# Kernel tuning notes

Hardware: AMD Instinct MI355X
Metric: run time of the kernel (lower is better)

The kernel has to match this reference:

```python
import jax, jax.numpy as jnp
import numpy as np
from jax import lax

DN = ('NCHW', 'OIHW', 'NCHW')
NUM_HEADS = 6


def _conv1x1(x, w):
    return lax.conv_general_dilated(x, w, (1, 1), 'VALID', dimension_numbers=DN)


def _dwconv3x3(x, w):
    # depthwise 3x3, groups == channels, padding 1
    return lax.conv_general_dilated(x, w, (1, 1), ((1, 1), (1, 1)),
                                    dimension_numbers=DN,
                                    feature_group_count=w.shape[0])


def setup_inputs() -> dict:
    key = jax.random.key(0)
    ks = jax.random.split(key, 7)
    b, dim, h, w = 4, 192, 128, 128
    inp = {
        'x': jax.random.normal(ks[0], (b, dim, h, w), jnp.float32),
        'ref': jax.random.normal(ks[1], (b, dim, h, w), jnp.float32),
        'w_qkv': jax.random.normal(ks[2], (dim * 3, dim, 1, 1), jnp.float32) * 0.05,
        'w_dw': jax.random.normal(ks[3], (dim * 3, 1, 3, 3), jnp.float32) * 0.1,
        'w_proj': jax.random.normal(ks[4], (dim, dim, 1, 1), jnp.float32) * 0.05,
        'temperature': jnp.ones((NUM_HEADS, 1, 1), jnp.float32),
        'attn_w': 0.2 * jnp.ones((4,), jnp.float32),
    }
    return inp


def reference(x, ref, w_qkv, w_dw, w_proj, temperature, attn_w):
    b, c, h, w = x.shape
    heads = NUM_HEADS
    C = c // heads  # per-head channel dim
    hw = h * w

    qkv = _dwconv3x3(_conv1x1(x, w_qkv), w_dw)        # [b, 3c, h, w]
    ref_qkv = _dwconv3x3(_conv1x1(ref, w_qkv), w_dw)  # shared weights

    q_shared = qkv[:, :c]            # q from x
    k_shared = ref_qkv[:, c:2 * c]   # k from ref
    v_shared = ref_qkv[:, 2 * c:]    # v from ref

    def to_heads(t):  # [b, c, h, w] -> [b, head, C, hw]
        return t.reshape(b, heads, C, hw)

    q = to_heads(q_shared)
    k = to_heads(k_shared)
    v = to_heads(v_shared)

    # L2-normalize along token dim (last axis)
    q = q / jnp.maximum(jnp.linalg.norm(q, axis=-1, keepdims=True), 1e-12)
    k = k / jnp.maximum(jnp.linalg.norm(k, axis=-1, keepdims=True), 1e-12)

    # channel-wise attention: [b, head, C, C]
    attn = jnp.einsum('bhcn,bhdn->bhcd', q, k) * temperature

    ks_list = [int(C / 2), int(C * 2 / 3), int(C * 3 / 4), int(C * 4 / 5)]
    neg_inf = jnp.asarray(-jnp.inf, attn.dtype)

    out = 0.0
    for i, ki in enumerate(ks_list):
        vals = lax.top_k(attn, ki)[0]            # [b, head, C, ki]
        thr = vals[..., -1:]                     # k-th largest per row
        a = jnp.where(attn >= thr, attn, neg_inf)
        a = jax.nn.softmax(a, axis=-1)
        out = out + attn_w[i] * jnp.einsum('bhcd,bhdn->bhcn', a, v)

    out = out.reshape(b, c, h, w)
    return _conv1x1(out, w_proj)
```

## Files before the change

kernel.cpp:

```cpp
#include <hip/hip_runtime.h>
#include <cstdint>
#include <cstddef>

typedef unsigned short u16;
typedef unsigned int u32;
typedef __attribute__((ext_vector_type(2))) float f32x2;
typedef __attribute__((ext_vector_type(4))) float f32x4;
typedef __attribute__((ext_vector_type(8))) short short8;
typedef __attribute__((ext_vector_type(2))) u32 u32x2;
typedef __attribute__((ext_vector_type(4))) u32 u32x4;

#define DEV static __device__ __forceinline__
#define HW 16384

DEV u16 f2bf(float f) {
  u32 u = __float_as_uint(f);
  u = (u + 0x7fffu + ((u >> 16) & 1u)) >> 16;
  return (u16)u;
}
DEV float bf2f(u16 h) { return __uint_as_float(((u32)h) << 16); }

DEV u32 packsplit(float f) {
  u16 h = f2bf(f);
  u16 l = f2bf(f - bf2f(h));
  return (u32)h | ((u32)l << 16);
}
DEV void unpack8(const u32* w, short8& hi, short8& lo) {
  #pragma unroll
  for (int i = 0; i < 8; ++i) {
    hi[i] = (short)(u16)w[i];
    lo[i] = (short)(u16)(w[i] >> 16);
  }
}
DEV void mfma3(f32x4& acc, short8 ah, short8 al, short8 bh, short8 bl) {
  acc = __builtin_amdgcn_mfma_f32_16x16x32_bf16(ah, bh, acc, 0, 0, 0);
  acc = __builtin_amdgcn_mfma_f32_16x16x32_bf16(ah, bl, acc, 0, 0, 0);
  acc = __builtin_amdgcn_mfma_f32_16x16x32_bf16(al, bh, acc, 0, 0, 0);
}


__global__ __launch_bounds__(256) void ksplit2(const float* __restrict__ in,
                                               u16* __restrict__ oh,
                                               u16* __restrict__ ol, int n) {
  int i = blockIdx.x * 256 + threadIdx.x;
  if (i >= n) return;
  int R = i / 192, K = i % 192;
  int halfblk = R / 96, rem = R % 96, mf = rem >> 4, r = rem & 15;
  int p = K >> 5, kk = K & 31, g = kk >> 3, j = kk & 7;
  size_t o16 = (((size_t)halfblk * 6 + p) * 6 + mf) * 512 + (size_t)(g * 16 + r) * 8 + j;
  float f = in[i];
  u16 h = f2bf(f);
  oh[o16] = h;
  ol[o16] = f2bf(f - bf2f(h));
}

template<int ABATCH, int BPACKED>
__global__ __launch_bounds__(512, 4) void gemm8(const u16* __restrict__ Afh,
                                                const u16* __restrict__ Afl,
                                                const u32* __restrict__ B0,
                                                const u32* __restrict__ B1,
                                                float* __restrict__ C0,
                                                float* __restrict__ C1) {
  __shared__ u32 Bs[2][128 * 34];
  const int t = threadIdx.x, lane = t & 63, wid = t >> 6;
  const int b = blockIdx.z, n0 = blockIdx.x * 128, y = blockIdx.y;
  const u32* Bb = (y == 0 ? B0 : B1) + (size_t)b * 192 * (size_t)HW;
  float* Cb = (y == 0) ? (C0 + (size_t)b * 192 * (size_t)HW)
                       : (C1 + ((size_t)b * 384 + (size_t)(y - 1) * 192) * (size_t)HW);
  const int wr = wid >> 2, wc = wid & 3;
  const int g = lane >> 4, r16 = lane & 15;
  const int bk = t >> 4;
  const int bn = t & 15;
  const int halfblk = (ABATCH ? b : y) * 2 + wr;
  const u16* Ah_w = Afh + (size_t)halfblk * 36 * 512 + (size_t)lane * 8;
  const u16* Al_w = Afl + (size_t)halfblk * 36 * 512 + (size_t)lane * 8;
  f32x4 acc[6][2] = {};

  u32 Breg[8], Bnext[8];
  #pragma unroll
  for (int j = 0; j < 8; ++j)
    Breg[j] = Bb[(size_t)bk * HW + n0 + bn + 16 * j];
  #pragma unroll 1
  for (int p = 0; p < 6; ++p) {
    u32* bufc = Bs[p & 1];
    #pragma unroll
    for (int j = 0; j < 8; ++j)
      bufc[(bn + 16 * j) * 34 + bk] =
          BPACKED ? Breg[j] : packsplit(__uint_as_float(Breg[j]));
    if (p < 5) {
      #pragma unroll
      for (int j = 0; j < 8; ++j)
        Bnext[j] = Bb[(size_t)((p + 1) * 32 + bk) * HW + n0 + bn + 16 * j];
    }
    __syncthreads();
    short8 bh[2], bl[2];
    #pragma unroll
    for (int nf = 0; nf < 2; ++nf) {
      u32 bw[8];
      const u32* bp = &bufc[(wc * 32 + nf * 16 + r16) * 34 + g * 8];
      *(u32x2*)&bw[0] = *(const u32x2*)&bp[0];
      *(u32x2*)&bw[2] = *(const u32x2*)&bp[2];
      *(u32x2*)&bw[4] = *(const u32x2*)&bp[4];
      *(u32x2*)&bw[6] = *(const u32x2*)&bp[6];
      unpack8(bw, bh[nf], bl[nf]);
    }
    #pragma unroll
    for (int mf = 0; mf < 6; ++mf) {
      const int fo = (p * 6 + mf) << 9;
      short8 ah = *(const short8*)(Ah_w + fo);
      short8 al = *(const short8*)(Al_w + fo);
      #pragma unroll
      for (int nf = 0; nf < 2; ++nf) {
        acc[mf][nf] = __builtin_amdgcn_mfma_f32_16x16x32_bf16(ah, bh[nf], acc[mf][nf], 0, 0, 0);
        acc[mf][nf] = __builtin_amdgcn_mfma_f32_16x16x32_bf16(ah, bl[nf], acc[mf][nf], 0, 0, 0);
        acc[mf][nf] = __builtin_amdgcn_mfma_f32_16x16x32_bf16(al, bh[nf], acc[mf][nf], 0, 0, 0);
      }
    }
    #pragma unroll
    for (int j = 0; j < 8; ++j) Breg[j] = Bnext[j];
  }
  #pragma unroll
  for (int mf = 0; mf < 6; ++mf)
    #pragma unroll
    for (int nf = 0; nf < 2; ++nf)
      #pragma unroll
      for (int rr = 0; rr < 4; ++rr)
        Cb[(size_t)(wr * 96 + mf * 16 + g * 4 + rr) * HW + n0 + wc * 32 + nf * 16 + r16] =
            acc[mf][nf][rr];
}

template<int SSQ>
__global__ __launch_bounds__(512) void k2_dw(const float* __restrict__ Tin, int cstIn,
                                             const float* __restrict__ wdw, int wco,
                                             u32* __restrict__ O,
                                             float* __restrict__ ssq, int sspath) {
  const int rt = blockIdx.x, cg = blockIdx.y, b = blockIdx.z;
  const int t = threadIdx.x, lane = t & 63, w = t >> 6;
  __shared__ float In[8][10][132];
  for (int idx = t; idx < 10400; idx += 512) {
    int ch = idx / 1300, rem = idx % 1300;
    int r = rem / 130, ci = rem % 130;
    int gr = rt * 8 + r - 1, gc = ci - 1;
    float v = 0.f;
    if (gr >= 0 && gr < 128 && gc >= 0 && gc < 128)
      v = Tin[((size_t)b * cstIn + cg * 8 + ch) * HW + gr * 128 + gc];
    In[ch][r][ci] = v;
  }
  float wv[9];
  #pragma unroll
  for (int j = 0; j < 9; ++j) wv[j] = wdw[(size_t)(wco + cg * 8 + w) * 9 + j];
  __syncthreads();
  float s = 0.f;
  u32* Op = O + ((size_t)b * 192 + cg * 8 + w) * HW + rt * 8 * 128 + 2 * lane;
  #pragma unroll
  for (int i = 0; i < 8; ++i) {
    float a0 = 0.f, a1 = 0.f;
    #pragma unroll
    for (int dr = 0; dr < 3; ++dr) {
      f32x2 u0 = *(const f32x2*)&In[w][i + dr][2 * lane];
      f32x2 u1 = *(const f32x2*)&In[w][i + dr][2 * lane + 2];
      a0 += wv[dr * 3] * u0[0] + wv[dr * 3 + 1] * u0[1] + wv[dr * 3 + 2] * u1[0];
      a1 += wv[dr * 3] * u0[1] + wv[dr * 3 + 1] * u1[0] + wv[dr * 3 + 2] * u1[1];
    }
    u32x2 o = {packsplit(a0), packsplit(a1)};
    *(u32x2*)&Op[(size_t)i * 128] = o;
    if (SSQ) s += a0 * a0 + a1 * a1;
  }
  if (SSQ) {
    #pragma unroll
    for (int off = 32; off; off >>= 1) s += __shfl_down(s, off);
    if (lane == 0) ssq[(((size_t)b * 2 + sspath) * 192 + cg * 8 + w) * 16 + rt] = s;
  }
}

__global__ __launch_bounds__(256) void k3_gram(const u32* __restrict__ q,
                                               const u32* __restrict__ k,
                                               float* __restrict__ gp) {
  const int ck = blockIdx.x, bh = blockIdx.y;
  const int b = bh / 6, h = bh % 6;
  const int t = threadIdx.x, lane = t & 63, wid = t >> 6;
  const int r16 = lane & 15, g = lane >> 4;
  const int chunk = ck * 4 + wid;
  const size_t rbase = ((size_t)b * 192 + h * 32 + r16) * HW;
  const u32* qp = q + rbase;
  const u32* kp = k + rbase;
  __shared__ float red[4][1024];
  f32x4 acc[2][2] = {};
  #pragma unroll 1
  for (int s = 0; s < 8; ++s) {
    int n = chunk * 256 + s * 32 + g * 8;
    u32 wq0[8], wq1[8], wk0[8], wk1[8];
    *(u32x4*)&wq0[0] = *(const u32x4*)&qp[n];
    *(u32x4*)&wq0[4] = *(const u32x4*)&qp[n + 4];
    *(u32x4*)&wq1[0] = *(const u32x4*)&qp[(size_t)16 * HW + n];
    *(u32x4*)&wq1[4] = *(const u32x4*)&qp[(size_t)16 * HW + n + 4];
    *(u32x4*)&wk0[0] = *(const u32x4*)&kp[n];
    *(u32x4*)&wk0[4] = *(const u32x4*)&kp[n + 4];
    *(u32x4*)&wk1[0] = *(const u32x4*)&kp[(size_t)16 * HW + n];
    *(u32x4*)&wk1[4] = *(const u32x4*)&kp[(size_t)16 * HW + n + 4];
    short8 a0h, a0l, a1h, a1l, b0h, b0l, b1h, b1l;
    unpack8(wq0, a0h, a0l);
    unpack8(wq1, a1h, a1l);
    unpack8(wk0, b0h, b0l);
    unpack8(wk1, b1h, b1l);
    mfma3(acc[0][0], a0h, a0l, b0h, b0l);
    mfma3(acc[0][1], a0h, a0l, b1h, b1l);
    mfma3(acc[1][0], a1h, a1l, b0h, b0l);
    mfma3(acc[1][1], a1h, a1l, b1h, b1l);
  }
  #pragma unroll
  for (int mf = 0; mf < 2; ++mf)
    #pragma unroll
    for (int nf = 0; nf < 2; ++nf)
      #pragma unroll
      for (int rr = 0; rr < 4; ++rr)
        red[wid][(mf * 16 + g * 4 + rr) * 32 + nf * 16 + r16] = acc[mf][nf][rr];
  __syncthreads();
  float* outp = gp + ((size_t)bh * 16 + ck) * 1024;
  #pragma unroll
  for (int e = t; e < 1024; e += 256)
    outp[e] = red[0][e] + red[1][e] + red[2][e] + red[3][e];
}

__global__ __launch_bounds__(512) void k4_comb(const float* __restrict__ gp,
                                               const float* __restrict__ ssq,
                                               const float* __restrict__ temp,
                                               const float* __restrict__ aw,
                                               const float* __restrict__ wproj,
                                               u16* __restrict__ mfh,
                                               u16* __restrict__ mfl) {
  const int bh = blockIdx.x, b = bh / 6, h = bh % 6;
  const int t = threadIdx.x;
  __shared__ float Gs[1024];
  __shared__ float Acm[1024];
  __shared__ float Wp[192 * 32];
  __shared__ float nq[32], nk[32];
  #pragma unroll
  for (int i = 0; i < 3; ++i) {
    int idx = t + i * 512;
    int row = idx >> 3, c4 = (idx & 7) << 2;
    *(f32x4*)&Wp[row * 32 + c4] = *(const f32x4*)&wproj[(size_t)row * 192 + h * 32 + c4];
  }
  {
    const float* p = gp + (size_t)bh * 16 * 1024 + 2 * t;
    f32x2 s = {};
    #pragma unroll
    for (int ch = 0; ch < 16; ++ch) {
      f32x2 v = *(const f32x2*)&p[(size_t)ch * 1024];
      s[0] += v[0]; s[1] += v[1];
    }
    *(f32x2*)&Gs[2 * t] = s;
  }
  if (t < 64) {
    int c = t & 31, pk = t >> 5;
    const float* sp = ssq + (((size_t)b * 2 + pk) * 192 + h * 32 + c) * 16;
    f32x4 s4 = {};
    #pragma unroll
    for (int i = 0; i < 4; ++i) {
      f32x4 v = *(const f32x4*)&sp[4 * i];
      s4[0] += v[0]; s4[1] += v[1]; s4[2] += v[2]; s4[3] += v[3];
    }
    float nr = fmaxf(sqrtf(s4[0] + s4[1] + s4[2] + s4[3]), 1e-12f);
    if (pk == 0) nq[c] = nr; else nk[c] = nr;
  }
  __syncthreads();
  const float T = temp[h];
  {
    int c = (2 * t) >> 5;
    f32x2 v = *(const f32x2*)&Gs[2 * t];
    float inq = T / nq[c];
    v[0] = v[0] * inq / nk[(2 * t) & 31];
    v[1] = v[1] * inq / nk[(2 * t + 1) & 31];
    __syncthreads();
    *(f32x2*)&Gs[2 * t] = v;
  }
  __syncthreads();
  const float aw0 = aw[0], aw1 = aw[1], aw2 = aw[2], aw3 = aw[3];
  const int half = t >> 5, d = t & 31;
  #pragma unroll
  for (int it = 0; it < 2; ++it) {
    const int c = it * 16 + half;
    const float v = Gs[c * 32 + d];
    int cnt = 0;
    #pragma unroll
    for (int dd = 0; dd < 32; ++dd) cnt += (Gs[c * 32 + dd] >= v) ? 1 : 0;
    float c0 = v;
    float c1 = (cnt >= 16) ? v : -3.0e38f;
    float c2 = (cnt >= 21) ? v : -3.0e38f;
    float c3 = (cnt >= 24) ? v : -3.0e38f;
    float c4 = (cnt >= 25) ? v : -3.0e38f;
    #pragma unroll
    for (int off = 16; off; off >>= 1) {
      c0 = fmaxf(c0, __shfl_xor(c0, off));
      c1 = fmaxf(c1, __shfl_xor(c1, off));
      c2 = fmaxf(c2, __shfl_xor(c2, off));
      c3 = fmaxf(c3, __shfl_xor(c3, off));
      c4 = fmaxf(c4, __shfl_xor(c4, off));
    }
    const float m = c0;
    const float ex = expf(v - m);
    float z1 = (v >= c1) ? ex : 0.f;
    float z2 = (v >= c2) ? ex : 0.f;
    float z3 = (v >= c3) ? ex : 0.f;
    float z4 = (v >= c4) ? ex : 0.f;
    #pragma unroll
    for (int off = 16; off; off >>= 1) {
      z1 += __shfl_xor(z1, off);
      z2 += __shfl_xor(z2, off);
      z3 += __shfl_xor(z3, off);
      z4 += __shfl_xor(z4, off);
    }
    float a = 0.f;
    a += (v >= c1) ? aw0 * ex / z1 : 0.f;
    a += (v >= c2) ? aw1 * ex / z2 : 0.f;
    a += (v >= c3) ? aw2 * ex / z3 : 0.f;
    a += (v >= c4) ? aw3 * ex / z4 : 0.f;
    Acm[c * 32 + d] = a;
  }
  __syncthreads();
  #pragma unroll
  for (int i = 0; i < 12; ++i) {
    int idx = t + i * 512;
    int co = idx >> 5, dd = idx & 31;
    float s = 0.f;
    #pragma unroll
    for (int c = 0; c < 32; ++c) s += Wp[co * 32 + c] * Acm[c * 32 + dd];
    int wr2 = co / 96, rem = co % 96, mf = rem >> 4, r = rem & 15;
    int lane2 = ((dd >> 3) << 4) + r, j = dd & 7;
    size_t o16 = ((((size_t)b * 2 + wr2) * 6 + h) * 6 + mf) * 512 + (size_t)lane2 * 8 + j;
    u16 hh = f2bf(s);
    mfh[o16] = hh;
    mfl[o16] = f2bf(s - bf2f(hh));
  }
}

extern "C" void kernel_launch(void* const* d_in, const int* in_sizes, int n_in,
                              void* d_out, int out_size, void* d_ws, size_t ws_size,
                              hipStream_t stream) {
  const float* x     = (const float*)d_in[0];
  const float* ref   = (const float*)d_in[1];
  const float* wqkv  = (const float*)d_in[2];
  const float* wdw   = (const float*)d_in[3];
  const float* wproj = (const float*)d_in[4];
  const float* temp  = (const float*)d_in[5];
  const float* aw    = (const float*)d_in[6];
  float* out = (float*)d_out;
  char* ws = (char*)d_ws;

  const size_t S = (size_t)4 * 192 * HW * 4;
  float* Ckv = (float*)(ws);
  float* Cq  = (float*)(ws + 2 * S);
  u32*   qpk = (u32*)(ws + 3 * S);
  char*  p5  = ws + 4 * S;
  float* gp  = (float*)(p5);
  float* ssq = (float*)(p5 + 1572864);
  u16*   afh = (u16*)(p5 + 1572864 + 98304);
  u16*   afl = (u16*)(p5 + 1572864 + 98304 + 221184);
  u16*   mfh = (u16*)(p5 + 1572864 + 98304 + 2 * 221184);
  u16*   mfl = (u16*)(p5 + 1572864 + 98304 + 2 * 221184 + 294912);
  u32*   kpk = (u32*)Cq;
  u32*   vpk = qpk;

  ksplit2<<<dim3(432), 256, 0, stream>>>(wqkv, afh, afl, 576 * 192);
  gemm8<0, 0><<<dim3(128, 3, 4), 512, 0, stream>>>(afh, afl, (const u32*)x,
                                                   (const u32*)ref, Cq, Ckv);
  k2_dw<1><<<dim3(16, 24, 4), 512, 0, stream>>>(Cq, 192, wdw, 0, qpk, ssq, 0);
  k2_dw<1><<<dim3(16, 24, 4), 512, 0, stream>>>(Ckv, 384, wdw, 192, kpk, ssq, 1);
  k3_gram<<<dim3(16, 24), 256, 0, stream>>>(qpk, kpk, gp);
  k2_dw<0><<<dim3(16, 24, 4), 512, 0, stream>>>(Ckv + (size_t)192 * HW, 384, wdw, 384,
                                                vpk, nullptr, 2);
  k4_comb<<<dim3(24), 512, 0, stream>>>(gp, ssq, temp, aw, wproj, mfh, mfl);
  gemm8<1, 1><<<dim3(128, 1, 4), 512, 0, stream>>>(mfh, mfl, vpk, vpk, out, out);
}
```

Before: 224.3 us.

## Load B fragments directly from global memory, dropping the LDS staging in the GEMM

After: 241.3 us. 7.6% more time.

```diff
diff --git a/kernel.cpp b/kernel.cpp
--- a/kernel.cpp
+++ b/kernel.cpp
@@ -55,13 +55,12 @@
 }
 
 template<int ABATCH, int BPACKED>
-__global__ __launch_bounds__(512, 4) void gemm8(const u16* __restrict__ Afh,
+__global__ __launch_bounds__(512, 4) void gemm9(const u16* __restrict__ Afh,
                                                 const u16* __restrict__ Afl,
                                                 const u32* __restrict__ B0,
                                                 const u32* __restrict__ B1,
                                                 float* __restrict__ C0,
                                                 float* __restrict__ C1) {
-  __shared__ u32 Bs[2][128 * 34];
   const int t = threadIdx.x, lane = t & 63, wid = t >> 6;
   const int b = blockIdx.z, n0 = blockIdx.x * 128, y = blockIdx.y;
   const u32* Bb = (y == 0 ? B0 : B1) + (size_t)b * 192 * (size_t)HW;
@@ -69,55 +68,48 @@
                        : (C1 + ((size_t)b * 384 + (size_t)(y - 1) * 192) * (size_t)HW);
   const int wr = wid >> 2, wc = wid & 3;
   const int g = lane >> 4, r16 = lane & 15;
-  const int bk = t >> 4;
-  const int bn = t & 15;
   const int halfblk = (ABATCH ? b : y) * 2 + wr;
   const u16* Ah_w = Afh + (size_t)halfblk * 36 * 512 + (size_t)lane * 8;
   const u16* Al_w = Afl + (size_t)halfblk * 36 * 512 + (size_t)lane * 8;
+  const u32* Bp0 = Bb + (size_t)(g * 8) * HW + n0 + wc * 32 + r16;
+  const u32* Bp1 = Bp0 + 16;
   f32x4 acc[6][2] = {};
 
-  u32 Breg[8], Bnext[8];
-  #pragma unroll
-  for (int j = 0; j < 8; ++j)
-    Breg[j] = Bb[(size_t)bk * HW + n0 + bn + 16 * j];
+  u32 bw0[8], bw1[8], bn0[8], bn1[8];
+  #pragma unroll
+  for (int j = 0; j < 8; ++j) {
+    bw0[j] = Bp0[(size_t)j * HW];
+    bw1[j] = Bp1[(size_t)j * HW];
+  }
   #pragma unroll 1
   for (int p = 0; p < 6; ++p) {
-    u32* bufc = Bs[p & 1];
-    #pragma unroll
-    for (int j = 0; j < 8; ++j)
-      bufc[(bn + 16 * j) * 34 + bk] =
-          BPACKED ? Breg[j] : packsplit(__uint_as_float(Breg[j]));
     if (p < 5) {
       #pragma unroll
-      for (int j = 0; j < 8; ++j)
-        Bnext[j] = Bb[(size_t)((p + 1) * 32 + bk) * HW + n0 + bn + 16 * j];
-    }
-    __syncthreads();
-    short8 bh[2], bl[2];
-    #pragma unroll
-    for (int nf = 0; nf < 2; ++nf) {
-      u32 bw[8];
-      const u32* bp = &bufc[(wc * 32 + nf * 16 + r16) * 34 + g * 8];
-      *(u32x2*)&bw[0] = *(const u32x2*)&bp[0];
-      *(u32x2*)&bw[2] = *(const u32x2*)&bp[2];
-      *(u32x2*)&bw[4] = *(const u32x2*)&bp[4];
-      *(u32x2*)&bw[6] = *(const u32x2*)&bp[6];
-      unpack8(bw, bh[nf], bl[nf]);
-    }
+      for (int j = 0; j < 8; ++j) {
+        bn0[j] = Bp0[(size_t)((p + 1) * 32 + j) * HW];
+        bn1[j] = Bp1[(size_t)((p + 1) * 32 + j) * HW];
+      }
+    }
+    if (!BPACKED) {
+      #pragma unroll
+      for (int j = 0; j < 8; ++j) {
+        bw0[j] = packsplit(__uint_as_float(bw0[j]));
+        bw1[j] = packsplit(__uint_as_float(bw1[j]));
+      }
+    }
+    short8 bh0, bl0, bh1, bl1;
+    unpack8(bw0, bh0, bl0);
+    unpack8(bw1, bh1, bl1);
     #pragma unroll
     for (int mf = 0; mf < 6; ++mf) {
       const int fo = (p * 6 + mf) << 9;
       short8 ah = *(const short8*)(Ah_w + fo);
       short8 al = *(const short8*)(Al_w + fo);
-      #pragma unroll
-      for (int nf = 0; nf < 2; ++nf) {
-        acc[mf][nf] = __builtin_amdgcn_mfma_f32_16x16x32_bf16(ah, bh[nf], acc[mf][nf], 0, 0, 0);
-        acc[mf][nf] = __builtin_amdgcn_mfma_f32_16x16x32_bf16(ah, bl[nf], acc[mf][nf], 0, 0, 0);
-        acc[mf][nf] = __builtin_amdgcn_mfma_f32_16x16x32_bf16(al, bh[nf], acc[mf][nf], 0, 0, 0);
-      }
-    }
-    #pragma unroll
-    for (int j = 0; j < 8; ++j) Breg[j] = Bnext[j];
+      mfma3(acc[mf][0], ah, al, bh0, bl0);
+      mfma3(acc[mf][1], ah, al, bh1, bl1);
+    }
+    #pragma unroll
+    for (int j = 0; j < 8; ++j) { bw0[j] = bn0[j]; bw1[j] = bn1[j]; }
   }
   #pragma unroll
   for (int mf = 0; mf < 6; ++mf)
@@ -362,7 +354,7 @@
   u32*   vpk = qpk;
 
   ksplit2<<<dim3(432), 256, 0, stream>>>(wqkv, afh, afl, 576 * 192);
-  gemm8<0, 0><<<dim3(128, 3, 4), 512, 0, stream>>>(afh, afl, (const u32*)x,
+  gemm9<0, 0><<<dim3(128, 3, 4), 512, 0, stream>>>(afh, afl, (const u32*)x,
                                                    (const u32*)ref, Cq, Ckv);
   k2_dw<1><<<dim3(16, 24, 4), 512, 0, stream>>>(Cq, 192, wdw, 0, qpk, ssq, 0);
   k2_dw<1><<<dim3(16, 24, 4), 512, 0, stream>>>(Ckv, 384, wdw, 192, kpk, ssq, 1);
@@ -370,5 +362,5 @@
   k2_dw<0><<<dim3(16, 24, 4), 512, 0, stream>>>(Ckv + (size_t)192 * HW, 384, wdw, 384,
                                                 vpk, nullptr, 2);
   k4_comb<<<dim3(24), 512, 0, stream>>>(gp, ssq, temp, aw, wproj, mfh, mfl);
-  gemm8<1, 1><<<dim3(128, 1, 4), 512, 0, stream>>>(mfh, mfl, vpk, vpk, out, out);
-}
+  gemm9<1, 1><<<dim3(128, 1, 4), 512, 0, stream>>>(mfh, mfl, vpk, vpk, out, out);
+}
```

## Use per-wave B staging in GEMM and merge q/k depthwise launches

Applied to the files above, without the earlier changes.

After: 254.3 us. 1.13x slower.

```diff
diff --git a/kernel.cpp b/kernel.cpp
--- a/kernel.cpp
+++ b/kernel.cpp
@@ -55,53 +55,47 @@
 }
 
 template<int ABATCH, int BPACKED>
-__global__ __launch_bounds__(512, 4) void gemm8(const u16* __restrict__ Afh,
-                                                const u16* __restrict__ Afl,
-                                                const u32* __restrict__ B0,
-                                                const u32* __restrict__ B1,
-                                                float* __restrict__ C0,
-                                                float* __restrict__ C1) {
-  __shared__ u32 Bs[2][128 * 34];
+__global__ __launch_bounds__(256, 4) void gemm12(const u16* __restrict__ Afh,
+                                                 const u16* __restrict__ Afl,
+                                                 const u32* __restrict__ B0,
+                                                 const u32* __restrict__ B1,
+                                                 float* __restrict__ C0,
+                                                 float* __restrict__ C1) {
+  __shared__ u32 Bls[4][2][1152];
   const int t = threadIdx.x, lane = t & 63, wid = t >> 6;
-  const int b = blockIdx.z, n0 = blockIdx.x * 128, y = blockIdx.y;
+  const int b = blockIdx.z, y = blockIdx.y;
+  const int wr = wid >> 1, wc = wid & 1;
+  const int n0w = blockIdx.x * 64 + wc * 32;
   const u32* Bb = (y == 0 ? B0 : B1) + (size_t)b * 192 * (size_t)HW;
   float* Cb = (y == 0) ? (C0 + (size_t)b * 192 * (size_t)HW)
                        : (C1 + ((size_t)b * 384 + (size_t)(y - 1) * 192) * (size_t)HW);
-  const int wr = wid >> 2, wc = wid & 3;
   const int g = lane >> 4, r16 = lane & 15;
-  const int bk = t >> 4;
-  const int bn = t & 15;
   const int halfblk = (ABATCH ? b : y) * 2 + wr;
   const u16* Ah_w = Afh + (size_t)halfblk * 36 * 512 + (size_t)lane * 8;
   const u16* Al_w = Afl + (size_t)halfblk * 36 * 512 + (size_t)lane * 8;
+  const int kk = lane >> 1, bhalf = lane & 1;
+  const u32* Bsrc = Bb + (size_t)kk * HW + n0w + 16 * bhalf;
   f32x4 acc[6][2] = {};
 
-  u32 Breg[8], Bnext[8];
-  #pragma unroll
-  for (int j = 0; j < 8; ++j)
-    Breg[j] = Bb[(size_t)bk * HW + n0 + bn + 16 * j];
-  #pragma unroll 1
+  #pragma unroll
   for (int p = 0; p < 6; ++p) {
-    u32* bufc = Bs[p & 1];
-    #pragma unroll
-    for (int j = 0; j < 8; ++j)
-      bufc[(bn + 16 * j) * 34 + bk] =
-          BPACKED ? Breg[j] : packsplit(__uint_as_float(Breg[j]));
-    if (p < 5) {
+    u32* sl = &Bls[wid][p & 1][0];
+    #pragma unroll
+    for (int j = 0; j < 4; ++j) {
+      u32x4 v = *(const u32x4*)(Bsrc + (size_t)(p * 32) * HW + 4 * j);
       #pragma unroll
-      for (int j = 0; j < 8; ++j)
-        Bnext[j] = Bb[(size_t)((p + 1) * 32 + bk) * HW + n0 + bn + 16 * j];
-    }
-    __syncthreads();
+      for (int i = 0; i < 4; ++i) {
+        u32 pw = BPACKED ? v[i] : packsplit(__uint_as_float(v[i]));
+        sl[(16 * bhalf + 4 * j + i) * 36 + kk] = pw;
+      }
+    }
     short8 bh[2], bl[2];
     #pragma unroll
     for (int nf = 0; nf < 2; ++nf) {
       u32 bw[8];
-      const u32* bp = &bufc[(wc * 32 + nf * 16 + r16) * 34 + g * 8];
-      *(u32x2*)&bw[0] = *(const u32x2*)&bp[0];
-      *(u32x2*)&bw[2] = *(const u32x2*)&bp[2];
-      *(u32x2*)&bw[4] = *(const u32x2*)&bp[4];
-      *(u32x2*)&bw[6] = *(const u32x2*)&bp[6];
+      const u32* rp = &sl[(nf * 16 + r16) * 36 + g * 8];
+      *(u32x4*)&bw[0] = *(const u32x4*)&rp[0];
+      *(u32x4*)&bw[4] = *(const u32x4*)&rp[4];
       unpack8(bw, bh[nf], bl[nf]);
     }
     #pragma unroll
@@ -109,15 +103,9 @@
       const int fo = (p * 6 + mf) << 9;
       short8 ah = *(const short8*)(Ah_w + fo);
       short8 al = *(const short8*)(Al_w + fo);
-      #pragma unroll
-      for (int nf = 0; nf < 2; ++nf) {
-        acc[mf][nf] = __builtin_amdgcn_mfma_f32_16x16x32_bf16(ah, bh[nf], acc[mf][nf], 0, 0, 0);
-        acc[mf][nf] = __builtin_amdgcn_mfma_f32_16x16x32_bf16(ah, bl[nf], acc[mf][nf], 0, 0, 0);
-        acc[mf][nf] = __builtin_amdgcn_mfma_f32_16x16x32_bf16(al, bh[nf], acc[mf][nf], 0, 0, 0);
-      }
-    }
-    #pragma unroll
-    for (int j = 0; j < 8; ++j) Breg[j] = Bnext[j];
+      mfma3(acc[mf][0], ah, al, bh[0], bl[0]);
+      mfma3(acc[mf][1], ah, al, bh[1], bl[1]);
+    }
   }
   #pragma unroll
   for (int mf = 0; mf < 6; ++mf)
@@ -125,27 +113,48 @@
     for (int nf = 0; nf < 2; ++nf)
       #pragma unroll
       for (int rr = 0; rr < 4; ++rr)
-        Cb[(size_t)(wr * 96 + mf * 16 + g * 4 + rr) * HW + n0 + wc * 32 + nf * 16 + r16] =
+        Cb[(size_t)(wr * 96 + mf * 16 + g * 4 + rr) * HW + n0w + nf * 16 + r16] =
             acc[mf][nf][rr];
 }
 
-template<int SSQ>
-__global__ __launch_bounds__(512) void k2_dw(const float* __restrict__ Tin, int cstIn,
-                                             const float* __restrict__ wdw, int wco,
-                                             u32* __restrict__ O,
-                                             float* __restrict__ ssq, int sspath) {
-  const int rt = blockIdx.x, cg = blockIdx.y, b = blockIdx.z;
+DEV void k2_stage(const float* __restrict__ src, int rt, int w, int lane,
+                  float (*In)[10][132]) {
+  #pragma unroll
+  for (int r = 0; r < 10; ++r) {
+    int gr = rt * 8 + r - 1;
+    bool rowok = (gr >= 0) && (gr < 128);
+    const float* rsrc = src + (size_t)gr * 128;
+    #pragma unroll
+    for (int j = 0; j < 2; ++j) {
+      int ci = j * 64 + lane;
+      int gc = ci - 1;
+      float v = (rowok && gc >= 0) ? rsrc[gc] : 0.f;
+      In[w][r][ci] = v;
+    }
+    if (lane < 2) {
+      float v = (rowok && lane == 0) ? rsrc[127] : 0.f;
+      In[w][r][128 + lane] = v;
+    }
+  }
+}
+
+__global__ __launch_bounds__(512) void k2qk(const float* __restrict__ Cq,
+                                            const float* __restrict__ Ckv,
+                                            const float* __restrict__ wdw,
+                                            u32* __restrict__ qpk,
+                                            u32* __restrict__ kpk,
+                                            float* __restrict__ ssq) {
+  const int rt = blockIdx.x, cgy = blockIdx.y, b = blockIdx.z;
   const int t = threadIdx.x, lane = t & 63, w = t >> 6;
+  const int isK = cgy >= 24;
+  const int cg = isK ? cgy - 24 : cgy;
+  const int cstIn = isK ? 384 : 192;
+  const int wco = isK ? 192 : 0;
+  const float* Tin = isK ? Ckv : Cq;
+  u32* O = isK ? kpk : qpk;
+  const int sspath = isK;
   __shared__ float In[8][10][132];
-  for (int idx = t; idx < 10400; idx += 512) {
-    int ch = idx / 1300, rem = idx % 1300;
-    int r = rem / 130, ci = rem % 130;
-    int gr = rt * 8 + r - 1, gc = ci - 1;
-    float v = 0.f;
-    if (gr >= 0 && gr < 128 && gc >= 0 && gc < 128)
-      v = Tin[((size_t)b * cstIn + cg * 8 + ch) * HW + gr * 128 + gc];
-    In[ch][r][ci] = v;
-  }
+  k2_stage(Tin + ((size_t)b * cstIn + cg * 8 + w) * HW, rt, w, lane, In);
   float wv[9];
   #pragma unroll
   for (int j = 0; j < 9; ++j) wv[j] = wdw[(size_t)(wco + cg * 8 + w) * 9 + j];
@@ -164,12 +173,37 @@
     }
     u32x2 o = {packsplit(a0), packsplit(a1)};
     *(u32x2*)&Op[(size_t)i * 128] = o;
-    if (SSQ) s += a0 * a0 + a1 * a1;
-  }
-  if (SSQ) {
-    #pragma unroll
-    for (int off = 32; off; off >>= 1) s += __shfl_down(s, off);
-    if (lane == 0) ssq[(((size_t)b * 2 + sspath) * 192 + cg * 8 + w) * 16 + rt] = s;
+    s += a0 * a0 + a1 * a1;
+  }
+  #pragma unroll
+  for (int off = 32; off; off >>= 1) s += __shfl_down(s, off);
+  if (lane == 0) ssq[(((size_t)b * 2 + sspath) * 192 + cg * 8 + w) * 16 + rt] = s;
+}
+
+__global__ __launch_bounds__(512) void k2v(const float* __restrict__ Tin,
+                                           const float* __restrict__ wdw,
+                                           u32* __restrict__ O) {
+  const int rt = blockIdx.x, cg = blockIdx.y, b = blockIdx.z;
+  const int t = threadIdx.x, lane = t & 63, w = t >> 6;
+  __shared__ float In[8][10][132];
+  k2_stage(Tin + ((size_t)b * 384 + cg * 8 + w) * HW, rt, w, lane, In);
+  float wv[9];
+  #pragma unroll
+  for (int j = 0; j < 9; ++j) wv[j] = wdw[(size_t)(384 + cg * 8 + w) * 9 + j];
+  __syncthreads();
+  u32* Op = O + ((size_t)b * 192 + cg * 8 + w) * HW + rt * 8 * 128 + 2 * lane;
+  #pragma unroll
+  for (int i = 0; i < 8; ++i) {
+    float a0 = 0.f, a1 = 0.f;
+    #pragma unroll
+    for (int dr = 0; dr < 3; ++dr) {
+      f32x2 u0 = *(const f32x2*)&In[w][i + dr][2 * lane];
+      f32x2 u1 = *(const f32x2*)&In[w][i + dr][2 * lane + 2];
+      a0 += wv[dr * 3] * u0[0] + wv[dr * 3 + 1] * u0[1] + wv[dr * 3 + 2] * u1[0];
+      a1 += wv[dr * 3] * u0[1] + wv[dr * 3 + 1] * u1[0] + wv[dr * 3 + 2] * u1[1];
+    }
+    u32x2 o = {packsplit(a0), packsplit(a1)};
+    *(u32x2*)&Op[(size_t)i * 128] = o;
   }
 }
 
@@ -358,17 +392,15 @@
   u16*   afl = (u16*)(p5 + 1572864 + 98304 + 221184);
   u16*   mfh = (u16*)(p5 + 1572864 + 98304 + 2 * 221184);
   u16*   mfl = (u16*)(p5 + 1572864 + 98304 + 2 * 221184 + 294912);
-  u32*   kpk = (u32*)Cq;
+  u32*   kpk = (u32*)d_out;
   u32*   vpk = qpk;
 
   ksplit2<<<dim3(432), 256, 0, stream>>>(wqkv, afh, afl, 576 * 192);
-  gemm8<0, 0><<<dim3(128, 3, 4), 512, 0, stream>>>(afh, afl, (const u32*)x,
-                                                   (const u32*)ref, Cq, Ckv);
-  k2_dw<1><<<dim3(16, 24, 4), 512, 0, stream>>>(Cq, 192, wdw, 0, qpk, ssq, 0);
-  k2_dw<1><<<dim3(16, 24, 4), 512, 0, stream>>>(Ckv, 384, wdw, 192, kpk, ssq, 1);
+  gemm12<0, 0><<<dim3(256, 3, 4), 256, 0, stream>>>(afh, afl, (const u32*)x,
+                                                    (const u32*)ref, Cq, Ckv);
+  k2qk<<<dim3(16, 48, 4), 512, 0, stream>>>(Cq, Ckv, wdw, qpk, kpk, ssq);
   k3_gram<<<dim3(16, 24), 256, 0, stream>>>(qpk, kpk, gp);
-  k2_dw<0><<<dim3(16, 24, 4), 512, 0, stream>>>(Ckv + (size_t)192 * HW, 384, wdw, 384,
-                                                vpk, nullptr, 2);
+  k2v<<<dim3(16, 24, 4), 512, 0, stream>>>(Ckv + (size_t)192 * HW, wdw, vpk);
   k4_comb<<<dim3(24), 512, 0, stream>>>(gp, ssq, temp, aw, wproj, mfh, mfl);
-  gemm8<1, 1><<<dim3(128, 1, 4), 512, 0, stream>>>(mfh, mfl, vpk, vpk, out, out);
-}
+  gemm12<1, 1><<<dim3(256, 1, 4), 256, 0, stream>>>(mfh, mfl, vpk, vpk, out, out);
+}
```
